# Kernel tuning notes

Hardware: AMD Instinct MI355X
Metric: run time of the kernel (lower is better)

The kernel has to match this reference:

```python
import jax, jax.numpy as jnp
import numpy as np

B, N, E = 4, 10000, 160000
F_EXOG = 8
IN_DIM = 9          # 1 (pm25) + F_EXOG
HIST, PRED = 8, 12
HID = 64
GNN_OUT = 13
E_HID, E_OUT = 32, 30
GRU_IN = IN_DIM + GNN_OUT  # 22


def setup_inputs() -> dict:
    key = jax.random.key(0)
    ks = jax.random.split(key, 16)
    s = 0.1
    return {
        "pm25_hist": jax.random.normal(ks[0], (B, HIST, N, 1), jnp.float32),
        "feature": jax.random.normal(ks[1], (B, HIST + PRED, N, F_EXOG), jnp.float32),
        "edge_attr": jax.random.uniform(ks[2], (E, 2), jnp.float32),
        "wind_mean": jnp.array([2.0, 180.0], jnp.float32),
        "wind_std": jnp.array([1.5, 90.0], jnp.float32),
        # edge MLP: Linear(21->32), Sigmoid, Linear(32->30), Sigmoid
        "e_w1": jax.random.normal(ks[3], (2 * IN_DIM + 3, E_HID), jnp.float32) * s,
        "e_b1": jnp.zeros((E_HID,), jnp.float32),
        "e_w2": jax.random.normal(ks[4], (E_HID, E_OUT), jnp.float32) * s,
        "e_b2": jnp.zeros((E_OUT,), jnp.float32),
        # node MLP: Linear(30->13), Sigmoid
        "n_w": jax.random.normal(ks[5], (E_OUT, GNN_OUT), jnp.float32) * s,
        "n_b": jnp.zeros((GNN_OUT,), jnp.float32),
        # GRUCell(22 -> 64), torch layout: weight_ih (3H, in), weight_hh (3H, H)
        "gru_wi": jax.random.normal(ks[6], (3 * HID, GRU_IN), jnp.float32) * s,
        "gru_wh": jax.random.normal(ks[7], (3 * HID, HID), jnp.float32) * s,
        "gru_bi": jnp.zeros((3 * HID,), jnp.float32),
        "gru_bh": jnp.zeros((3 * HID,), jnp.float32),
        # fc_out: Linear(64 -> 1)
        "fc_w": jax.random.normal(ks[8], (HID, 1), jnp.float32) * s,
        "fc_b": jnp.zeros((1,), jnp.float32),
        "edge_index": jax.random.randint(ks[9], (2, E), 0, N, jnp.int64),
    }


def _forward(pm25_hist, feature, edge_attr, wind_mean, wind_std,
             e_w1, e_b1, e_w2, e_b2, n_w, n_b,
             gru_wi, gru_wh, gru_bi, gru_bh, fc_w, fc_b, edge_index):
    batch, _, n_nodes, _ = pm25_hist.shape
    src, tgt = edge_index[0], edge_index[1]

    # buffers precomputed in __init__ (torch.std uses ddof=1)
    edge_mean = edge_attr.mean(axis=0, keepdims=True)
    edge_std = jnp.maximum(jnp.std(edge_attr, axis=0, ddof=1, keepdims=True), 1e-6)
    edge_attr_norm = (edge_attr - edge_mean) / edge_std          # (E, 2)
    city_dist = jnp.maximum(edge_attr[:, 0], 1e-3)               # (E,)
    city_direc = edge_attr[:, 1]                                 # (E,)
    w_std = jnp.maximum(wind_std, 1e-6)

    def graph_gnn(x):                                            # x: (B, N, IN_DIM)
        node_src = x[:, src]                                     # (B, E, IN_DIM)
        node_tgt = x[:, tgt]
        wind = node_src[..., -2:] * w_std + wind_mean            # de-normalize
        speed = jnp.maximum(wind[..., 0], 0.0)                   # (B, E)
        wdir = jnp.deg2rad(wind[..., 1])
        theta = jnp.abs(city_direc - wdir)
        edge_w = jax.nn.relu(3.0 * speed * jnp.cos(theta) / city_dist)  # (B, E)
        ean = jnp.broadcast_to(edge_attr_norm, (x.shape[0], E, 2))
        h = jnp.concatenate([node_src, node_tgt, ean, edge_w[..., None]], axis=-1)
        h = jax.nn.sigmoid(h @ e_w1 + e_b1)
        h = jax.nn.sigmoid(h @ e_w2 + e_b2)                      # (B, E, E_OUT)
        agg = jnp.zeros((x.shape[0], n_nodes, E_OUT), x.dtype)
        agg = agg.at[:, tgt].add(h).at[:, src].add(-h)           # scatter add / sub
        return jax.nn.sigmoid(agg @ n_w + n_b)                   # (B, N, GNN_OUT)

    def gru_step(h, x):                                          # h,x: (B*N, .)
        gi = x @ gru_wi.T + gru_bi
        gh = h @ gru_wh.T + gru_bh
        i_r, i_z, i_n = jnp.split(gi, 3, axis=-1)
        h_r, h_z, h_n = jnp.split(gh, 3, axis=-1)
        r = jax.nn.sigmoid(i_r + h_r)
        z = jax.nn.sigmoid(i_z + h_z)
        n = jnp.tanh(i_n + r * h_n)
        return (1.0 - z) * n + z * h

    def step(carry, feat_t):
        hn, xn = carry                                           # (B*N,HID), (B,N,1)
        x = jnp.concatenate([xn, feat_t], axis=-1)               # (B, N, IN_DIM)
        x_gnn = graph_gnn(x)
        xc = jnp.concatenate([x_gnn, x], axis=-1).reshape(batch * n_nodes, -1)
        hn = gru_step(hn, xc)
        xn = hn.reshape(batch, n_nodes, HID) @ fc_w + fc_b       # (B, N, 1)
        return (hn, xn), xn[..., 0]

    hn0 = jnp.zeros((batch * n_nodes, HID), pm25_hist.dtype)
    xn0 = pm25_hist[:, -1]                                       # (B, N, 1)
    feats = jnp.swapaxes(feature[:, HIST:HIST + PRED], 0, 1)     # (PRED, B, N, F)
    _, preds = jax.lax.scan(step, (hn0, xn0), feats)             # (PRED, B, N)
    return jnp.transpose(preds, (1, 2, 0))                       # (B, N, PRED)


def reference(pm25_hist, feature, edge_attr, wind_mean, wind_std,
              e_w1, e_b1, e_w2, e_b2, n_w, n_b,
              gru_wi, gru_wh, gru_bi, gru_bh, fc_w, fc_b, edge_index):
    return _forward(pm25_hist, feature, edge_attr, wind_mean, wind_std,
                    e_w1, e_b1, e_w2, e_b2, n_w, n_b,
                    gru_wi, gru_wh, gru_bi, gru_bh, fc_w, fc_b, edge_index)
```

## Files before the change

### kernel.cpp

```cpp
#include <hip/hip_runtime.h>
#include <hip/hip_fp16.h>
#include <cstddef>

#define BB    4
#define NN    10000
#define EE    160000
#define BN    40000
#define HISTC 8
#define PREDC 12
#define TSTEP 20
#define FEX   8
#define HIDC  64
#define EHID  32
#define EOUTC 30
#define GOUTC 13
#define GINC  22

typedef float v2f __attribute__((ext_vector_type(2)));
typedef _Float16 v2h __attribute__((ext_vector_type(2)));

struct alignas(16) WPack {
    __half2 w[16];
    float   nw[14];
    float   b2;
    float   pad;
};

__device__ __forceinline__ float fast_rcp(float x) { return __builtin_amdgcn_rcpf(x); }
__device__ __forceinline__ float sigm(float x) {
    return fast_rcp(1.0f + __expf(-x));
}
__device__ __forceinline__ v2f sigm2(v2f x) {
    v2f r; r.x = sigm(x.x); r.y = sigm(x.y); return r;
}
__device__ __forceinline__ float tanh_fast(float x) {
    x = fminf(fmaxf(x, -15.0f), 15.0f);
    float e = __expf(2.0f * x);
    return (e - 1.0f) * fast_rcp(e + 1.0f);
}

__device__ __forceinline__ float dot2(__half2 a, __half2 b, float c) {
#if __has_builtin(__builtin_amdgcn_fdot2)
    union { __half2 h; v2h v; } ua, ub;
    ua.h = a; ub.h = b;
    return __builtin_amdgcn_fdot2(ua.v, ub.v, c, false);
#else
    float2 fa = __half22float2(a), fb = __half22float2(b);
    return c + fa.x * fb.x + fa.y * fb.y;
#endif
}

__global__ __launch_bounds__(256) void stats1_kernel(const float* __restrict__ ea,
                                                     double* __restrict__ part) {
    __shared__ double sm[256][4];
    int tid = threadIdx.x;
    double s0 = 0, s1 = 0, q0 = 0, q1 = 0;
    for (int e = blockIdx.x * 256 + tid; e < EE; e += 256 * 256) {
        float2 v = reinterpret_cast<const float2*>(ea)[e];
        double v0 = (double)v.x, v1 = (double)v.y;
        s0 += v0; q0 += v0 * v0;
        s1 += v1; q1 += v1 * v1;
    }
    sm[tid][0] = s0; sm[tid][1] = s1; sm[tid][2] = q0; sm[tid][3] = q1;
    __syncthreads();
    for (int off = 128; off > 0; off >>= 1) {
        if (tid < off)
            for (int k = 0; k < 4; k++) sm[tid][k] += sm[tid + off][k];
        __syncthreads();
    }
    if (tid == 0) {
        part[blockIdx.x * 4 + 0] = sm[0][0];
        part[blockIdx.x * 4 + 1] = sm[0][1];
        part[blockIdx.x * 4 + 2] = sm[0][2];
        part[blockIdx.x * 4 + 3] = sm[0][3];
    }
}

__global__ __launch_bounds__(256) void stats2_kernel(const double* __restrict__ part,
                                                     float* __restrict__ stats) {
    __shared__ double sm[256][4];
    int tid = threadIdx.x;
    sm[tid][0] = part[tid * 4 + 0];
    sm[tid][1] = part[tid * 4 + 1];
    sm[tid][2] = part[tid * 4 + 2];
    sm[tid][3] = part[tid * 4 + 3];
    __syncthreads();
    for (int off = 128; off > 0; off >>= 1) {
        if (tid < off)
            for (int k = 0; k < 4; k++) sm[tid][k] += sm[tid + off][k];
        __syncthreads();
    }
    if (tid == 0) {
        double m0 = sm[0][0] / EE, m1 = sm[0][1] / EE;
        double v0 = (sm[0][2] - sm[0][0] * sm[0][0] / EE) / (double)(EE - 1);
        double v1 = (sm[0][3] - sm[0][1] * sm[0][1] / EE) / (double)(EE - 1);
        float sd0 = fmaxf((float)sqrt(v0 > 0 ? v0 : 0.0), 1e-6f);
        float sd1 = fmaxf((float)sqrt(v1 > 0 ? v1 : 0.0), 1e-6f);
        stats[0] = (float)m0; stats[1] = (float)m1;
        stats[2] = 1.0f / sd0; stats[3] = 1.0f / sd1;
    }
}

__global__ __launch_bounds__(256) void edgepre_kernel(
    const float* __restrict__ ea, const float* __restrict__ stats,
    float4* __restrict__ epre4)
{
    int e = blockIdx.x * 256 + threadIdx.x;
    if (e >= EE) return;
    float2 v = reinterpret_cast<const float2*>(ea)[e];
    float4 r;
    r.x = (v.x - stats[0]) * stats[2];
    r.y = (v.y - stats[1]) * stats[3];
    r.z = 1.0f / fmaxf(v.x, 1e-3f);
    r.w = v.y;
    epre4[e] = r;
}

__global__ __launch_bounds__(256) void cvtw_kernel(
    const float* __restrict__ wi, const float* __restrict__ wh,
    const float* __restrict__ ew2, const float* __restrict__ eb2,
    const float* __restrict__ nw,
    __half* __restrict__ wi_h, __half* __restrict__ wh_h,
    WPack* __restrict__ wpack)
{
    int i = blockIdx.x * 256 + threadIdx.x;
    if (i < 192 * GINC) wi_h[i] = __float2half(wi[i]);
    if (i < 192 * HIDC) wh_h[i] = __float2half(wh[i]);
    if (i < EOUTC) {
        WPack wp;
        #pragma unroll
        for (int q = 0; q < 16; q++)
            wp.w[q] = __floats2half2_rn(ew2[(2 * q) * EOUTC + i],
                                        ew2[(2 * q + 1) * EOUTC + i]);
        #pragma unroll
        for (int j = 0; j < GOUTC; j++) wp.nw[j] = nw[i * GOUTC + j];
        wp.nw[13] = 0.f;
        wp.b2 = eb2[i];
        wp.pad = 0.f;
        wpack[i] = wp;
    }
}

__global__ void initxn_kernel(const float* __restrict__ pm, float* __restrict__ xn) {
    int i = blockIdx.x * 256 + threadIdx.x;
    if (i >= BN) return;
    int b = i / NN, n = i - b * NN;
    xn[i] = pm[(b * HISTC + (HISTC - 1)) * NN + n];
}

__global__ void hist_kernel(const int* __restrict__ eidx,
                            int* __restrict__ deg_t, int* __restrict__ deg_s) {
    int e = blockIdx.x * 256 + threadIdx.x;
    if (e >= EE) return;
    atomicAdd(&deg_s[eidx[e]], 1);
    atomicAdd(&deg_t[eidx[EE + e]], 1);
}

__global__ __launch_bounds__(1024) void scan_kernel(
    const int* __restrict__ deg_t, const int* __restrict__ deg_s,
    int* __restrict__ off_t, int* __restrict__ off_s,
    int* __restrict__ cnt_t, int* __restrict__ cnt_s)
{
    __shared__ int pt[1024], ps[1024];
    int tid = threadIdx.x;
    int base = tid * 10;
    int st = 0, ss = 0;
    for (int k = 0; k < 10; k++) {
        int i = base + k;
        if (i < NN) { st += deg_t[i]; ss += deg_s[i]; }
    }
    pt[tid] = st; ps[tid] = ss;
    __syncthreads();
    for (int off = 1; off < 1024; off <<= 1) {
        int vt = (tid >= off) ? pt[tid - off] : 0;
        int vs = (tid >= off) ? ps[tid - off] : 0;
        __syncthreads();
        pt[tid] += vt; ps[tid] += vs;
        __syncthreads();
    }
    int ext = (tid == 0) ? 0 : pt[tid - 1];
    int exs = (tid == 0) ? 0 : ps[tid - 1];
    for (int k = 0; k < 10; k++) {
        int i = base + k;
        if (i < NN) {
            off_t[i] = ext; cnt_t[i] = ext;
            off_s[i] = exs; cnt_s[i] = exs;
            ext += deg_t[i]; exs += deg_s[i];
        }
    }
    if (tid == 0) { off_t[NN] = EE; off_s[NN] = EE; }
}

__global__ void fill_kernel(const int* __restrict__ eidx,
                            int* __restrict__ cnt_t, int* __restrict__ cnt_s,
                            int4* __restrict__ epos)
{
    int e = blockIdx.x * 256 + threadIdx.x;
    if (e >= EE) return;
    int s = eidx[e];
    int g = eidx[EE + e];
    int pt = atomicAdd(&cnt_t[g], 1);
    int ps = atomicAdd(&cnt_s[s], 1);
    int4 r; r.x = s; r.y = g; r.z = pt; r.w = ps;
    epos[e] = r;
}

__global__ void perm_kernel(const int4* __restrict__ epos,
                            const float4* __restrict__ epre4,
                            int4* __restrict__ eT, float4* __restrict__ epreT)
{
    int e = blockIdx.x * 256 + threadIdx.x;
    if (e >= EE) return;
    int4 p = epos[e];
    int slot = p.z;
    int4 r; r.x = p.x; r.y = p.y; r.z = p.w; r.w = 0;
    eT[slot] = r;
    epreT[slot] = epre4[e];
}

__global__ __launch_bounds__(256) void pre_kernel(
    float* __restrict__ xncur, const float* __restrict__ feature, int t,
    const float* __restrict__ xp, const float* __restrict__ fb,
    const float* __restrict__ ew1,
    const float* __restrict__ wmean, const float* __restrict__ wstd,
    __half* __restrict__ preS, __half* __restrict__ preT,
    float2* __restrict__ wind2, float* __restrict__ out)
{
    __shared__ alignas(16) float w1s[18 * EHID];
    for (int i = threadIdx.x; i < 18 * EHID; i += 256) w1s[i] = ew1[i];
    __syncthreads();
    int idx = blockIdx.x * 256 + threadIdx.x;
    if (idx >= BN * 8) return;
    int i = idx >> 3;
    int c = idx & 7;
    int b = i / NN, n = i - b * NN;
    float x0;
    if (t == 0) {
        x0 = xncur[i];
    } else {
        x0 = xp[i] + xp[BN + i] + fb[0];
        if (c == 0) {
            xncur[i] = x0;
            out[(size_t)i * PREDC + (t - 1)] = x0;
        }
    }
    float x[9];
    x[0] = x0;
    {
        const float4* fp = reinterpret_cast<const float4*>(
            feature + (((size_t)b * TSTEP + HISTC + t) * NN + n) * FEX);
        float4 u = fp[0], v = fp[1];
        x[1] = u.x; x[2] = u.y; x[3] = u.z; x[4] = u.w;
        x[5] = v.x; x[6] = v.y; x[7] = v.z; x[8] = v.w;
    }
    float4 aS = {0.f, 0.f, 0.f, 0.f}, aT = {0.f, 0.f, 0.f, 0.f};
    #pragma unroll
    for (int k = 0; k < 9; k++) {
        float4 wS = reinterpret_cast<const float4*>(&w1s[k * EHID])[c];
        float4 wT = reinterpret_cast<const float4*>(&w1s[(9 + k) * EHID])[c];
        aS.x += x[k] * wS.x; aS.y += x[k] * wS.y; aS.z += x[k] * wS.z; aS.w += x[k] * wS.w;
        aT.x += x[k] * wT.x; aT.y += x[k] * wT.y; aT.z += x[k] * wT.z; aT.w += x[k] * wT.w;
    }
    union { uint2 u; __half h[4]; } sv, tv;
    sv.h[0] = __float2half(aS.x); sv.h[1] = __float2half(aS.y);
    sv.h[2] = __float2half(aS.z); sv.h[3] = __float2half(aS.w);
    tv.h[0] = __float2half(aT.x); tv.h[1] = __float2half(aT.y);
    tv.h[2] = __float2half(aT.z); tv.h[3] = __float2half(aT.w);
    reinterpret_cast<uint2*>(preS + (size_t)i * EHID)[c] = sv.u;
    reinterpret_cast<uint2*>(preT + (size_t)i * EHID)[c] = tv.u;
    if (c == 1) {
        float sd0 = fmaxf(wstd[0], 1e-6f), sd1 = fmaxf(wstd[1], 1e-6f);
        float speed = fmaxf(x[7] * sd0 + wmean[0], 0.f);
        float wdir  = (x[8] * sd1 + wmean[1]) * 0.017453292519943295f;
        float2 wv; wv.x = 3.0f * speed; wv.y = wdir;
        wind2[i] = wv;
    }
}

__global__ __launch_bounds__(256) void finalout_kernel(
    const float* __restrict__ xp, const float* __restrict__ fb,
    float* __restrict__ out)
{
    int i = blockIdx.x * 256 + threadIdx.x;
    if (i >= BN) return;
    out[(size_t)i * PREDC + (PREDC - 1)] = xp[i] + xp[BN + i] + fb[0];
}

__global__ __launch_bounds__(256) void edge_kernel(
    const int4* __restrict__ eT, const float4* __restrict__ epreT,
    const __half* __restrict__ preS, const __half* __restrict__ preT,
    const float2* __restrict__ wind2,
    const float* __restrict__ ew1, const float* __restrict__ eb1,
    const WPack* __restrict__ wpack,
    __half* __restrict__ h3t, __half* __restrict__ h3s)
{
    int i = blockIdx.x * 256 + threadIdx.x;
    int bA = blockIdx.y;
    int bB = bA + 2;
    int4 et = eT[i];
    int s = et.x, g = et.y, ps = et.z;
    float4 ep = epreT[i];

    size_t iSA = (size_t)bA * NN + s, iTA = (size_t)bA * NN + g;
    size_t iSB = (size_t)bB * NN + s, iTB = (size_t)bB * NN + g;
    float2 wA = wind2[iSA];
    float2 wB = wind2[iSB];
    v2f ew;
    ew.x = fmaxf(wA.x * __cosf(fabsf(ep.w - wA.y)) * ep.z, 0.f);
    ew.y = fmaxf(wB.x * __cosf(fabsf(ep.w - wB.y)) * ep.z, 0.f);

    union alignas(16) { uint4 u[4]; __half2 h2[16]; } RSA, RTA, RSB, RTB;
    {
        const uint4* p;
        p = reinterpret_cast<const uint4*>(preS + iSA * EHID);
        RSA.u[0] = p[0]; RSA.u[1] = p[1]; RSA.u[2] = p[2]; RSA.u[3] = p[3];
        p = reinterpret_cast<const uint4*>(preT + iTA * EHID);
        RTA.u[0] = p[0]; RTA.u[1] = p[1]; RTA.u[2] = p[2]; RTA.u[3] = p[3];
        p = reinterpret_cast<const uint4*>(preS + iSB * EHID);
        RSB.u[0] = p[0]; RSB.u[1] = p[1]; RSB.u[2] = p[2]; RSB.u[3] = p[3];
        p = reinterpret_cast<const uint4*>(preT + iTB * EHID);
        RTB.u[0] = p[0]; RTB.u[1] = p[1]; RTB.u[2] = p[2]; RTB.u[3] = p[3];
    }

    const v2f* W18 = reinterpret_cast<const v2f*>(ew1 + 18 * EHID);
    const v2f* W19 = reinterpret_cast<const v2f*>(ew1 + 19 * EHID);
    const v2f* W20 = reinterpret_cast<const v2f*>(ew1 + 20 * EHID);
    const v2f* B1  = reinterpret_cast<const v2f*>(eb1);
    float ean0 = ep.x, ean1 = ep.y;
    __half2 h1A[16], h1B[16];
    #pragma unroll
    for (int q = 0; q < 16; q++) {
        v2f base = W18[q] * ean0 + W19[q] * ean1 + B1[q];
        v2f w20q = W20[q];
        float2 rsA = __half22float2(RSA.h2[q]);
        float2 rtA = __half22float2(RTA.h2[q]);
        float2 rsB = __half22float2(RSB.h2[q]);
        float2 rtB = __half22float2(RTB.h2[q]);
        v2f uA, uB;
        uA.x = base.x + rsA.x + rtA.x + w20q.x * ew.x;
        uA.y = base.y + rsA.y + rtA.y + w20q.y * ew.x;
        uB.x = base.x + rsB.x + rtB.x + w20q.x * ew.y;
        uB.y = base.y + rsB.y + rtB.y + w20q.y * ew.y;
        v2f sA = sigm2(uA), sB = sigm2(uB);
        h1A[q] = __floats2half2_rn(sA.x, sA.y);
        h1B[q] = __floats2half2_rn(sB.x, sB.y);
    }

    v2f h3ab[GOUTC];
    #pragma unroll
    for (int j = 0; j < GOUTC; j++) { h3ab[j].x = 0.f; h3ab[j].y = 0.f; }
    for (int o = 0; o < EOUTC; o++) {
        const WPack* W = wpack + o;
        float accA = W->b2, accB = W->b2;
        #pragma unroll
        for (int q = 0; q < 16; q++) {
            __half2 wq = W->w[q];
            accA = dot2(h1A[q], wq, accA);
            accB = dot2(h1B[q], wq, accB);
        }
        v2f h2ab; h2ab.x = sigm(accA); h2ab.y = sigm(accB);
        #pragma unroll
        for (int j = 0; j < GOUTC; j++) h3ab[j] += W->nw[j] * h2ab;
    }

    union alignas(16) { uint4 u[2]; __half h[16]; } rA, rB;
    #pragma unroll
    for (int j = 0; j < GOUTC; j++) {
        rA.h[j] = __float2half(h3ab[j].x);
        rB.h[j] = __float2half(h3ab[j].y);
    }
    #pragma unroll
    for (int j = GOUTC; j < 16; j++) { rA.h[j] = __float2half(0.f); rB.h[j] = __float2half(0.f); }
    {
        __half* oT = h3t + ((size_t)bA * EE + i) * 16;
        reinterpret_cast<uint4*>(oT)[0] = rA.u[0];
        reinterpret_cast<uint4*>(oT)[1] = rA.u[1];
        oT = h3t + ((size_t)bB * EE + i) * 16;
        reinterpret_cast<uint4*>(oT)[0] = rB.u[0];
        reinterpret_cast<uint4*>(oT)[1] = rB.u[1];
        __half* oS = h3s + ((size_t)bA * EE + ps) * 16;
        reinterpret_cast<uint4*>(oS)[0] = rA.u[0];
        reinterpret_cast<uint4*>(oS)[1] = rA.u[1];
        oS = h3s + ((size_t)bB * EE + ps) * 16;
        reinterpret_cast<uint4*>(oS)[0] = rB.u[0];
        reinterpret_cast<uint4*>(oS)[1] = rB.u[1];
    }
}

__global__ __launch_bounds__(256) void gather_kernel(
    const __half* __restrict__ h3t, const __half* __restrict__ h3s,
    const int* __restrict__ off_t, const int* __restrict__ off_s,
    float* __restrict__ agg)
{
    int n = (blockIdx.x * 256 + threadIdx.x) >> 6;
    if (n >= NN) return;
    n = __builtin_amdgcn_readfirstlane(n);
    int lane = threadIdx.x & 63;
    int b = lane >> 4, ch = lane & 15;
    const __half* ht = h3t + (size_t)b * EE * 16 + ch;
    const __half* hs = h3s + (size_t)b * EE * 16 + ch;
    float a0 = 0.f, a1 = 0.f, a2 = 0.f, a3 = 0.f;
    {
        int i0 = off_t[n], i1 = off_t[n + 1];
        int i = i0;
        for (; i + 4 <= i1; i += 4) {
            a0 += __half2float(ht[(size_t)(i + 0) * 16]);
            a1 += __half2float(ht[(size_t)(i + 1) * 16]);
            a2 += __half2float(ht[(size_t)(i + 2) * 16]);
            a3 += __half2float(ht[(size_t)(i + 3) * 16]);
        }
        for (; i < i1; i++) a0 += __half2float(ht[(size_t)i * 16]);
    }
    {
        int i0 = off_s[n], i1 = off_s[n + 1];
        int i = i0;
        for (; i + 4 <= i1; i += 4) {
            a0 -= __half2float(hs[(size_t)(i + 0) * 16]);
            a1 -= __half2float(hs[(size_t)(i + 1) * 16]);
            a2 -= __half2float(hs[(size_t)(i + 2) * 16]);
            a3 -= __half2float(hs[(size_t)(i + 3) * 16]);
        }
        for (; i < i1; i++) a0 -= __half2float(hs[(size_t)i * 16]);
    }
    agg[((size_t)b * NN + n) * 16 + ch] = (a0 + a1) + (a2 + a3);
}

__global__ __launch_bounds__(256) void node_kernel(
    const float* __restrict__ xncur, const float* __restrict__ feature, int t,
    const float* __restrict__ agg, const float* __restrict__ nb,
    const __half* __restrict__ wi_h, const __half* __restrict__ wh_h,
    const float* __restrict__ bi, const float* __restrict__ bh,
    const float* __restrict__ fw,
    const __half2* __restrict__ hnold, __half2* __restrict__ hnnew,
    float* __restrict__ xp)
{
    __shared__ float xpart[4][64];
    int lane = threadIdx.x & 63;
    int wav  = threadIdx.x >> 6;
    int jb   = blockIdx.y;
    int node = blockIdx.x * 64 + lane;
    int b = node / NN;
    int n = node - b * NN;

    float xc[GINC];
    {
        const float4* ar = reinterpret_cast<const float4*>(agg + (size_t)node * 16);
        float4 a0 = ar[0], a1 = ar[1], a2 = ar[2];
        float a3 = agg[(size_t)node * 16 + 12];
        xc[0] = sigm(a0.x + nb[0]);  xc[1] = sigm(a0.y + nb[1]);
        xc[2] = sigm(a0.z + nb[2]);  xc[3] = sigm(a0.w + nb[3]);
        xc[4] = sigm(a1.x + nb[4]);  xc[5] = sigm(a1.y + nb[5]);
        xc[6] = sigm(a1.z + nb[6]);  xc[7] = sigm(a1.w + nb[7]);
        xc[8] = sigm(a2.x + nb[8]);  xc[9] = sigm(a2.y + nb[9]);
        xc[10] = sigm(a2.z + nb[10]); xc[11] = sigm(a2.w + nb[11]);
        xc[12] = sigm(a3 + nb[12]);
    }
    xc[13] = xncur[node];
    {
        const float4* fp = reinterpret_cast<const float4*>(
            feature + (((size_t)b * TSTEP + HISTC + t) * NN + n) * FEX);
        float4 u = fp[0], v = fp[1];
        xc[14] = u.x; xc[15] = u.y; xc[16] = u.z; xc[17] = u.w;
        xc[18] = v.x; xc[19] = v.y; xc[20] = v.z; xc[21] = v.w;
    }
    __half2 xch[11];
    #pragma unroll
    for (int p = 0; p < 11; p++) xch[p] = __floats2half2_rn(xc[2*p], xc[2*p+1]);

    __half2 hh[32];
    #pragma unroll
    for (int p = 0; p < 32; p++) hh[p] = hnold[(size_t)p * BN + node];

    float xsum = 0.f;
    #pragma unroll
    for (int jj2 = 0; jj2 < 4; jj2++) {
        int j0 = __builtin_amdgcn_readfirstlane(jb * 32 + wav * 8 + jj2 * 2);
        union { __half2 h; __half v[2]; } holdw;
        holdw.h = hnold[(size_t)(j0 >> 1) * BN + node];
        float hnew2[2];
        #pragma unroll
        for (int d = 0; d < 2; d++) {
            int j = j0 + d;
            float ir = bi[j], iz = bi[64 + j], in_ = bi[128 + j];
            const __half2* wr0 = reinterpret_cast<const __half2*>(wi_h + (size_t)j * GINC);
            const __half2* wr1 = reinterpret_cast<const __half2*>(wi_h + (size_t)(64 + j) * GINC);
            const __half2* wr2 = reinterpret_cast<const __half2*>(wi_h + (size_t)(128 + j) * GINC);
            #pragma unroll
            for (int p = 0; p < 11; p++) {
                ir  = dot2(xch[p], wr0[p], ir);
                iz  = dot2(xch[p], wr1[p], iz);
                in_ = dot2(xch[p], wr2[p], in_);
            }
            float hr = bh[j], hz = bh[64 + j], hn_ = bh[128 + j];
            const __half2* vr0 = reinterpret_cast<const __half2*>(wh_h + (size_t)j * HIDC);
            const __half2* vr1 = reinterpret_cast<const __half2*>(wh_h + (size_t)(64 + j) * HIDC);
            const __half2* vr2 = reinterpret_cast<const __half2*>(wh_h + (size_t)(128 + j) * HIDC);
            #pragma unroll
            for (int p = 0; p < 32; p++) {
                hr  = dot2(hh[p], vr0[p], hr);
                hz  = dot2(hh[p], vr1[p], hz);
                hn_ = dot2(hh[p], vr2[p], hn_);
            }
            float r  = sigm(ir + hr);
            float z  = sigm(iz + hz);
            float nn = tanh_fast(in_ + r * hn_);
            float hold = __half2float(holdw.v[d]);
            float hnew = (1.f - z) * nn + z * hold;
            hnew2[d] = hnew;
            xsum += hnew * fw[j];
        }
        hnnew[(size_t)(j0 >> 1) * BN + node] = __floats2half2_rn(hnew2[0], hnew2[1]);
    }
    xpart[wav][lane] = xsum;
    __syncthreads();
    if (wav == 0) {
        float tot = xpart[0][lane] + xpart[1][lane] + xpart[2][lane] + xpart[3][lane];
        xp[(size_t)jb * BN + node] = tot;
    }
}

extern "C" void kernel_launch(void* const* d_in, const int* in_sizes, int n_in,
                              void* d_out, int out_size, void* d_ws, size_t ws_size,
                              hipStream_t stream)
{
    const float* pm    = (const float*)d_in[0];
    const float* feat  = (const float*)d_in[1];
    const float* ea    = (const float*)d_in[2];
    const float* wmean = (const float*)d_in[3];
    const float* wstd  = (const float*)d_in[4];
    const float* ew1   = (const float*)d_in[5];
    const float* eb1   = (const float*)d_in[6];
    const float* ew2   = (const float*)d_in[7];
    const float* eb2   = (const float*)d_in[8];
    const float* nw    = (const float*)d_in[9];
    const float* nb    = (const float*)d_in[10];
    const float* wi    = (const float*)d_in[11];
    const float* wh    = (const float*)d_in[12];
    const float* bi    = (const float*)d_in[13];
    const float* bh    = (const float*)d_in[14];
    const float* fw    = (const float*)d_in[15];
    const float* fb    = (const float*)d_in[16];
    const int*   eidx  = (const int*)d_in[17];
    float* out = (float*)d_out;

    char* w = (char*)d_ws;
    double* partd = (double*)w;                    w += 256 * 4 * sizeof(double);
    float*  stats = (float*)w;                     w += 16 * sizeof(float);
    WPack*  wpack = (WPack*)w;                     w += EOUTC * sizeof(WPack);
    float4* epre4 = (float4*)w;                    w += (size_t)EE * sizeof(float4);
    float4* epreT = (float4*)w;                    w += (size_t)EE * sizeof(float4);
    float*  xncur = (float*)w;                     w += (size_t)BN * sizeof(float);
    float*  xp    = (float*)w;                     w += (size_t)2 * BN * sizeof(float);
    __half2* hnA  = (__half2*)w;                   w += (size_t)32 * BN * sizeof(__half2);
    __half2* hnB  = (__half2*)w;                   w += (size_t)32 * BN * sizeof(__half2);
    float*  agg13 = (float*)w;                     w += (size_t)BN * 16 * sizeof(float);
    __half* preS  = (__half*)w;                    w += (size_t)BN * EHID * sizeof(__half);
    __half* preT  = (__half*)w;                    w += (size_t)BN * EHID * sizeof(__half);
    float2* wind2 = (float2*)w;                    w += (size_t)BN * sizeof(float2);
    __half* h3t   = (__half*)w;                    w += (size_t)BB * EE * 16 * sizeof(__half);
    __half* h3s   = (__half*)w;                    w += (size_t)BB * EE * 16 * sizeof(__half);
    __half* wi_h  = (__half*)w;                    w += (size_t)192 * GINC * sizeof(__half);
    __half* wh_h  = (__half*)w;                    w += (size_t)192 * HIDC * sizeof(__half);
    int*    deg_t = (int*)w;                       w += NN * sizeof(int);
    int*    deg_s = (int*)w;                       w += NN * sizeof(int);
    int*    off_t = (int*)w;                       w += (NN + 1) * sizeof(int);
    int*    off_s = (int*)w;                       w += (NN + 1) * sizeof(int);
    int*    cnt_t = (int*)w;                       w += NN * sizeof(int);
    int*    cnt_s = (int*)w;                       w += NN * sizeof(int);
    int4*   epos  = (int4*)w;                      w += (size_t)EE * sizeof(int4);
    int4*   eT    = (int4*)w;                      w += (size_t)EE * sizeof(int4);

    stats1_kernel<<<256, 256, 0, stream>>>(ea, partd);
    stats2_kernel<<<1, 256, 0, stream>>>(partd, stats);
    edgepre_kernel<<<(EE + 255) / 256, 256, 0, stream>>>(ea, stats, epre4);
    cvtw_kernel<<<(192 * HIDC + 255) / 256, 256, 0, stream>>>(
        wi, wh, ew2, eb2, nw, wi_h, wh_h, wpack);
    initxn_kernel<<<(BN + 255) / 256, 256, 0, stream>>>(pm, xncur);
    hipMemsetAsync(hnA, 0, (size_t)32 * BN * sizeof(__half2), stream);
    hipMemsetAsync(deg_t, 0, 2 * NN * sizeof(int), stream);
    hist_kernel<<<(EE + 255) / 256, 256, 0, stream>>>(eidx, deg_t, deg_s);
    scan_kernel<<<1, 1024, 0, stream>>>(deg_t, deg_s, off_t, off_s, cnt_t, cnt_s);
    fill_kernel<<<(EE + 255) / 256, 256, 0, stream>>>(eidx, cnt_t, cnt_s, epos);
    perm_kernel<<<(EE + 255) / 256, 256, 0, stream>>>(epos, epre4, eT, epreT);

    for (int t = 0; t < PREDC; t++) {
        const __half2* hnold = (t & 1) ? hnB : hnA;
        __half2*       hnnew = (t & 1) ? hnA : hnB;
        pre_kernel<<<(BN * 8 + 255) / 256, 256, 0, stream>>>(
            xncur, feat, t, xp, fb, ew1, wmean, wstd, preS, preT, wind2, out);
        edge_kernel<<<dim3(EE / 256, 2), 256, 0, stream>>>(
            eT, epreT, preS, preT, wind2, ew1, eb1, wpack, h3t, h3s);
        gather_kernel<<<(NN * 64 + 255) / 256, 256, 0, stream>>>(
            h3t, h3s, off_t, off_s, agg13);
        node_kernel<<<dim3(BN / 64, 2), 256, 0, stream>>>(
            xncur, feat, t, agg13, nb, wi_h, wh_h, bi, bh, fw, hnold, hnnew, xp);
    }
    finalout_kernel<<<(BN + 255) / 256, 256, 0, stream>>>(xp, fb, out);
}
```

Measured before the change: 1.124 ms.

## Split GRU hidden units across four block columns and break dot-product dependency chains

The node kernel grid doubles along y, so each thread computes 4 instead of 8 hidden units. The fc partial sums therefore grow from 2 to 4 slices, which pre_kernel and finalout_kernel now add together. Both the edge MLP second layer and the GRU hidden matvec use two independent accumulators to shorten the dot2 dependency chains. The cost is that every node-kernel block must reload the hidden state and input features, doubling those redundant reads.

```diff
diff --git a/kernel.cpp b/kernel.cpp
--- a/kernel.cpp
+++ b/kernel.cpp
@@ -220,7 +220,8 @@
 
 __global__ __launch_bounds__(256) void pre_kernel(
     float* __restrict__ xncur, const float* __restrict__ feature, int t,
-    const float* __restrict__ xp, const float* __restrict__ fb,
+    const float* __restrict__ xp,
+    const float* __restrict__ fb,
     const float* __restrict__ ew1,
     const float* __restrict__ wmean, const float* __restrict__ wstd,
     __half* __restrict__ preS, __half* __restrict__ preT,
@@ -238,7 +239,7 @@
     if (t == 0) {
         x0 = xncur[i];
     } else {
-        x0 = xp[i] + xp[BN + i] + fb[0];
+        x0 = (xp[i] + xp[BN + i]) + (xp[2 * BN + i] + xp[3 * BN + i]) + fb[0];
         if (c == 0) {
             xncur[i] = x0;
             out[(size_t)i * PREDC + (t - 1)] = x0;
@@ -283,7 +284,8 @@
 {
     int i = blockIdx.x * 256 + threadIdx.x;
     if (i >= BN) return;
-    out[(size_t)i * PREDC + (PREDC - 1)] = xp[i] + xp[BN + i] + fb[0];
+    out[(size_t)i * PREDC + (PREDC - 1)] =
+        (xp[i] + xp[BN + i]) + (xp[2 * BN + i] + xp[3 * BN + i]) + fb[0];
 }
 
 __global__ __launch_bounds__(256) void edge_kernel(
@@ -351,14 +353,17 @@
     for (int j = 0; j < GOUTC; j++) { h3ab[j].x = 0.f; h3ab[j].y = 0.f; }
     for (int o = 0; o < EOUTC; o++) {
         const WPack* W = wpack + o;
-        float accA = W->b2, accB = W->b2;
+        float accA0 = W->b2, accA1 = 0.f;
+        float accB0 = W->b2, accB1 = 0.f;
         #pragma unroll
-        for (int q = 0; q < 16; q++) {
-            __half2 wq = W->w[q];
-            accA = dot2(h1A[q], wq, accA);
-            accB = dot2(h1B[q], wq, accB);
+        for (int q = 0; q < 16; q += 2) {
+            __half2 w0 = W->w[q], w1 = W->w[q + 1];
+            accA0 = dot2(h1A[q],     w0, accA0);
+            accB0 = dot2(h1B[q],     w0, accB0);
+            accA1 = dot2(h1A[q + 1], w1, accA1);
+            accB1 = dot2(h1B[q + 1], w1, accB1);
         }
-        v2f h2ab; h2ab.x = sigm(accA); h2ab.y = sigm(accB);
+        v2f h2ab; h2ab.x = sigm(accA0 + accA1); h2ab.y = sigm(accB0 + accB1);
         #pragma unroll
         for (int j = 0; j < GOUTC; j++) h3ab[j] += W->nw[j] * h2ab;
     }
@@ -473,8 +478,8 @@
 
     float xsum = 0.f;
     #pragma unroll
-    for (int jj2 = 0; jj2 < 4; jj2++) {
-        int j0 = __builtin_amdgcn_readfirstlane(jb * 32 + wav * 8 + jj2 * 2);
+    for (int jj2 = 0; jj2 < 2; jj2++) {
+        int j0 = __builtin_amdgcn_readfirstlane(jb * 16 + wav * 4 + jj2 * 2);
         union { __half2 h; __half v[2]; } holdw;
         holdw.h = hnold[(size_t)(j0 >> 1) * BN + node];
         float hnew2[2];
@@ -491,19 +496,23 @@
                 iz  = dot2(xch[p], wr1[p], iz);
                 in_ = dot2(xch[p], wr2[p], in_);
             }
-            float hr = bh[j], hz = bh[64 + j], hn_ = bh[128 + j];
+            float hr0 = bh[j], hz0 = bh[64 + j], hn0 = bh[128 + j];
+            float hr1 = 0.f, hz1 = 0.f, hn1 = 0.f;
             const __half2* vr0 = reinterpret_cast<const __half2*>(wh_h + (size_t)j * HIDC);
             const __half2* vr1 = reinterpret_cast<const __half2*>(wh_h + (size_t)(64 + j) * HIDC);
             const __half2* vr2 = reinterpret_cast<const __half2*>(wh_h + (size_t)(128 + j) * HIDC);
             #pragma unroll
-            for (int p = 0; p < 32; p++) {
-                hr  = dot2(hh[p], vr0[p], hr);
-                hz  = dot2(hh[p], vr1[p], hz);
-                hn_ = dot2(hh[p], vr2[p], hn_);
+            for (int p = 0; p < 32; p += 2) {
+                hr0 = dot2(hh[p],     vr0[p],     hr0);
+                hz0 = dot2(hh[p],     vr1[p],     hz0);
+                hn0 = dot2(hh[p],     vr2[p],     hn0);
+                hr1 = dot2(hh[p + 1], vr0[p + 1], hr1);
+                hz1 = dot2(hh[p + 1], vr1[p + 1], hz1);
+                hn1 = dot2(hh[p + 1], vr2[p + 1], hn1);
             }
-            float r  = sigm(ir + hr);
-            float z  = sigm(iz + hz);
-            float nn = tanh_fast(in_ + r * hn_);
+            float r  = sigm(ir + hr0 + hr1);
+            float z  = sigm(iz + hz0 + hz1);
+            float nn = tanh_fast(in_ + r * (hn0 + hn1));
             float hold = __half2float(holdw.v[d]);
             float hnew = (1.f - z) * nn + z * hold;
             hnew2[d] = hnew;
@@ -550,7 +559,7 @@
     float4* epre4 = (float4*)w;                    w += (size_t)EE * sizeof(float4);
     float4* epreT = (float4*)w;                    w += (size_t)EE * sizeof(float4);
     float*  xncur = (float*)w;                     w += (size_t)BN * sizeof(float);
-    float*  xp    = (float*)w;                     w += (size_t)2 * BN * sizeof(float);
+    float*  xp    = (float*)w;                     w += (size_t)4 * BN * sizeof(float);
     __half2* hnA  = (__half2*)w;                   w += (size_t)32 * BN * sizeof(__half2);
     __half2* hnB  = (__half2*)w;                   w += (size_t)32 * BN * sizeof(__half2);
     float*  agg13 = (float*)w;                     w += (size_t)BN * 16 * sizeof(float);
@@ -592,7 +601,7 @@
             eT, epreT, preS, preT, wind2, ew1, eb1, wpack, h3t, h3s);
         gather_kernel<<<(NN * 64 + 255) / 256, 256, 0, stream>>>(
             h3t, h3s, off_t, off_s, agg13);
-        node_kernel<<<dim3(BN / 64, 2), 256, 0, stream>>>(
+        node_kernel<<<dim3(BN / 64, 4), 256, 0, stream>>>(
             xncur, feat, t, agg13, nb, wi_h, wh_h, bi, bh, fw, hnold, hnnew, xp);
     }
     finalout_kernel<<<(BN + 255) / 256, 256, 0, stream>>>(xp, fb, out);
```

Result: faster. 1.069 ms (-4.9%).
